# Kernel optimization log

Hardware: AMD Instinct MI355X
Metric: run time of the kernel (lower is better)

Reference implementation:

```python
import jax, jax.numpy as jnp
import numpy as np

G = 128        # number of graphs
N = 512        # nodes per graph
F_IN = 128     # n_feat
H = 128        # agg_hidden
L = 5          # n_layer
FC = 128       # fc_hidden
C = 10         # n_class
E_HALF = 8192  # undirected edge pairs per graph (symmetrized -> 16384 directed)


def setup_inputs() -> dict:
    key = jax.random.key(0)
    ks = jax.random.split(key, 8)
    x = jax.random.normal(ks[0], (G * N, F_IN), dtype=jnp.float32)
    # per-graph random edges, offset into the block-diagonal node index space
    s = jax.random.randint(ks[1], (G, E_HALF), 0, N)
    d = jax.random.randint(ks[2], (G, E_HALF), 0, N)
    off = (jnp.arange(G) * N)[:, None]
    s = (s + off).reshape(-1)
    d = (d + off).reshape(-1)
    src = jnp.concatenate([s, d])  # symmetric adjacency (edges + reversed)
    dst = jnp.concatenate([d, s])
    eps = jnp.zeros((L,), jnp.float32)  # nn.Parameter(torch.zeros(n_layer))
    W = jax.random.normal(ks[3], (L, H, H), jnp.float32) / jnp.sqrt(H)
    b = jnp.zeros((L, H), jnp.float32)
    fc1_w = jax.random.normal(ks[4], (H, FC), jnp.float32) / jnp.sqrt(H)
    fc1_b = jnp.zeros((FC,), jnp.float32)
    fc2_w = jax.random.normal(ks[5], (FC, C), jnp.float32) / jnp.sqrt(FC)
    fc2_b = jnp.zeros((C,), jnp.float32)
    return {"x": x, "eps": eps, "W": W, "b": b,
            "fc1_w": fc1_w, "fc1_b": fc1_b, "fc2_w": fc2_w, "fc2_b": fc2_b,
            "src": src, "dst": dst}


def reference(x, eps, W, b, fc1_w, fc1_b, fc2_w, fc2_b, src, dst):
    n = x.shape[0]
    h = x
    for i in range(L):
        # sparse Adj @ h : gather along src, scatter-add to dst
        pooled = jax.ops.segment_sum(h[src], dst, num_segments=n)
        h = jax.nn.relu(((1.0 + eps[i]) * h + pooled) @ W[i] + b[i])
        # dropout p=0.0 / eval mode -> identity
    hg = h.reshape(G, N, -1).sum(axis=1)          # sum readout over nodes
    hg = jax.nn.relu(hg @ fc1_w + fc1_b)
    return jax.nn.softmax(hg @ fc2_w + fc2_b, axis=-1)
```

## Files before the change

kernel.cpp:

```cpp
#include <hip/hip_runtime.h>

#define NODES 65536
#define GNUM  128
#define NPG   512
#define FDIM  128

#define OFF_A   0u
#define OFF_WT  (16u<<20)
#define OFF_HTA (17u<<20)
#define OFF_HTB (33u<<20)

typedef short bf16x8 __attribute__((ext_vector_type(8)));
typedef float f32x4  __attribute__((ext_vector_type(4)));
typedef unsigned short u16;

#define GLB_AS __attribute__((address_space(1)))
#define LDS_AS __attribute__((address_space(3)))

static __device__ inline void gload16(const void* g, void* l) {
    __builtin_amdgcn_global_load_lds((const GLB_AS unsigned*)g,
                                     (LDS_AS unsigned*)l, 16, 0, 0);
}

static __device__ inline unsigned bf1(float x) {
    unsigned b = __float_as_uint(x);
    return (b + 0x7fffu + ((b >> 16) & 1u)) >> 16;
}
static __device__ inline unsigned pack_bf2(float x, float y) {
    return bf1(x) | (bf1(y) << 16);
}
static __device__ inline bf16x8 cvt8n(unsigned x) {
    union { bf16x8 v; unsigned u[4]; } r;
#pragma unroll
    for (int i = 0; i < 4; ++i) {
        float f0 = (float)((x >> (8 * i)) & 0xFu);
        float f1 = (float)((x >> (8 * i + 4)) & 0xFu);
        r.u[i] = (__float_as_uint(f0) >> 16) | (__float_as_uint(f1) & 0xffff0000u);
    }
    return r.v;
}

__global__ __launch_bounds__(256) void k_cvtT(const float* __restrict__ x,
                                              u16* __restrict__ hT) {
    __shared__ char Cs[128 * 144];
    int t = threadIdx.x;
    int m0 = blockIdx.x * 64;
    int g = m0 >> 9, ml0 = m0 & 511;
#pragma unroll
    for (int it = 0; it < 8; ++it) {
        int i = t + 256 * it;
        int nl = i >> 5, fq = i & 31;
        float4 v = *(const float4*)(x + (size_t)(m0 + nl) * FDIM + fq * 4);
        *(u16*)(Cs + (fq * 4 + 0) * 144 + nl * 2) = (u16)bf1(v.x);
        *(u16*)(Cs + (fq * 4 + 1) * 144 + nl * 2) = (u16)bf1(v.y);
        *(u16*)(Cs + (fq * 4 + 2) * 144 + nl * 2) = (u16)bf1(v.z);
        *(u16*)(Cs + (fq * 4 + 3) * 144 + nl * 2) = (u16)bf1(v.w);
    }
    __syncthreads();
    u16* hg = hT + (size_t)g * 65536 + ml0;
#pragma unroll
    for (int j = 0; j < 4; ++j) {
        int idx = t + 256 * j;
        int f = idx >> 3, piece = idx & 7;
        uint4 v = *(const uint4*)(Cs + f * 144 + piece * 16);
        *(uint4*)((char*)(hg + (size_t)f * 512) + piece * 16) = v;
    }
}

__global__ __launch_bounds__(256) void k_wt(const float* __restrict__ W,
                                            u16* __restrict__ wt) {
    int idx = blockIdx.x * 256 + threadIdx.x;
    int l = idx >> 14, r = idx & 16383;
    int n = r >> 7, k = r & 127;
    wt[idx] = (u16)bf1(W[(l << 14) + k * 128 + n]);
}

__global__ __launch_bounds__(512) void k_adense(const int* __restrict__ src,
                                                const int* __restrict__ dst,
                                                unsigned* __restrict__ A4,
                                                int halfE) {
    __shared__ unsigned cnt[128 * 64];
    int g = blockIdx.x >> 2, dq = blockIdx.x & 3;
    int t = threadIdx.x;
    for (int i = t; i < 128 * 64; i += 512) cnt[i] = 0u;
    __syncthreads();
    int dlo = dq * 128;
    int epg = halfE / GNUM;
#pragma unroll
    for (int r = 0; r < 2; ++r) {
        int base = r * halfE + g * epg;
        const int4* s4 = (const int4*)(src + base);
        const int4* d4 = (const int4*)(dst + base);
        for (int i = t; i < epg / 4; i += 512) {
            int4 sv = s4[i], dv = d4[i];
            int s, dl;
            s = sv.x & (NPG - 1); dl = (dv.x & (NPG - 1)) - dlo;
            if ((unsigned)dl < 128u) atomicAdd(&cnt[dl * 64 + (s >> 3)], 1u << ((s & 7) * 4));
            s = sv.y & (NPG - 1); dl = (dv.y & (NPG - 1)) - dlo;
            if ((unsigned)dl < 128u) atomicAdd(&cnt[dl * 64 + (s >> 3)], 1u << ((s & 7) * 4));
            s = sv.z & (NPG - 1); dl = (dv.z & (NPG - 1)) - dlo;
            if ((unsigned)dl < 128u) atomicAdd(&cnt[dl * 64 + (s >> 3)], 1u << ((s & 7) * 4));
            s = sv.w & (NPG - 1); dl = (dv.w & (NPG - 1)) - dlo;
            if ((unsigned)dl < 128u) atomicAdd(&cnt[dl * 64 + (s >> 3)], 1u << ((s & 7) * 4));
        }
    }
    __syncthreads();
    uint4* Ao = (uint4*)(A4 + ((size_t)g * 512 + dlo) * 64);
    const uint4* ls = (const uint4*)cnt;
    for (int i = t; i < 128 * 16; i += 512) Ao[i] = ls[i];
}

__global__ __launch_bounds__(512, 4) void k_layer(const u16* __restrict__ hT,
                                                  u16* __restrict__ hTo,
                                                  const unsigned char* __restrict__ A,
                                                  const u16* __restrict__ wt,
                                                  const float* __restrict__ bias,
                                                  const float* __restrict__ eps) {
    __shared__ uint4 smem16[75776 / 16];
    char* smem = (char*)smem16;
    char* Ps = smem + 40960;
    int t = threadIdx.x;
    int w = t >> 6, lane = t & 63;
    int q = lane >> 4, ln = lane & 15;
    int g = blockIdx.x & 127, dq = blockIdx.x >> 7;
    const unsigned char* Ab = A + (size_t)g * (512 * 256) + (size_t)dq * 128 * 256;
    const u16* hb = hT + (size_t)g * 65536;

    int pA = w * 64 + lane;
    int rowA = pA >> 1;
    const unsigned char* gA = Ab + rowA * 256 + (pA & 1) * 16;
    int pB0 = w * 128 + lane, pB1 = pB0 + 64;
    int fB0 = pB0 >> 3, fB1 = pB1 >> 3;
    const char* gB0 = (const char*)hb + (size_t)fB0 * 1024 + (((pB0 & 7) ^ (fB0 & 7)) << 4);
    const char* gB1 = (const char*)hb + (size_t)fB1 * 1024 + (((pB1 & 7) ^ (fB1 & 7)) << 4);

    f32x4 acc[8];
#pragma unroll
    for (int nt = 0; nt < 8; ++nt) acc[nt] = (f32x4){0.f, 0.f, 0.f, 0.f};

    int rA = w * 16 + ln;
    if (w < 4) gload16(gA, smem + pA * 16);
    gload16(gB0, smem + 8192 + pB0 * 16);
    gload16(gB1, smem + 8192 + pB1 * 16);
    __syncthreads();
    for (int ch = 0; ch < 8; ++ch) {
        char* Asc = smem + (ch & 1) * 4096;
        char* Bsc = smem + 8192 + (ch & 1) * 16384;
        if (ch < 7) {
            char* Asn = smem + ((ch + 1) & 1) * 4096;
            char* Bsn = smem + 8192 + ((ch + 1) & 1) * 16384;
            if (w < 4) gload16(gA + (ch + 1) * 32, Asn + pA * 16);
            gload16(gB0 + (ch + 1) * 128, Bsn + pB0 * 16);
            gload16(gB1 + (ch + 1) * 128, Bsn + pB1 * 16);
        }
#pragma unroll
        for (int kcL = 0; kcL < 2; ++kcL) {
            unsigned a4 = *(const unsigned*)(Asc + rA * 32 + kcL * 16 + q * 4);
            bf16x8 af = cvt8n(a4);
#pragma unroll
            for (int nt = 0; nt < 8; ++nt) {
                int f = nt * 16 + ln;
                int sB = f * 8 + ((kcL * 4 + q) ^ (f & 7));
                bf16x8 bf = *(const bf16x8*)(Bsc + sB * 16);
                acc[nt] = __builtin_amdgcn_mfma_f32_16x16x32_bf16(af, bf, acc[nt], 0, 0, 0);
            }
        }
        __syncthreads();
    }
    float ep = 1.f + eps[0];
    int rl0 = w * 16 + q * 4;
    int mb0 = dq * 128 + rl0;
#pragma unroll
    for (int nt = 0; nt < 8; ++nt) {
        int f = nt * 16 + ln;
        uint2 sv = *(const uint2*)(hb + (size_t)f * 512 + mb0);
        float s0 = __uint_as_float(sv.x << 16);
        float s1 = __uint_as_float(sv.x & 0xffff0000u);
        float s2 = __uint_as_float(sv.y << 16);
        float s3 = __uint_as_float(sv.y & 0xffff0000u);
        f32x4 a = acc[nt];
        *(u16*)(Ps + (rl0 + 0) * 272 + f * 2) = (u16)bf1(fmaf(ep, s0, a[0]));
        *(u16*)(Ps + (rl0 + 1) * 272 + f * 2) = (u16)bf1(fmaf(ep, s1, a[1]));
        *(u16*)(Ps + (rl0 + 2) * 272 + f * 2) = (u16)bf1(fmaf(ep, s2, a[2]));
        *(u16*)(Ps + (rl0 + 3) * 272 + f * 2) = (u16)bf1(fmaf(ep, s3, a[3]));
    }
    __syncthreads();
    f32x4 acc2[8];
#pragma unroll
    for (int nt = 0; nt < 8; ++nt) acc2[nt] = (f32x4){0.f, 0.f, 0.f, 0.f};
#pragma unroll
    for (int ks = 0; ks < 4; ++ks) {
        bf16x8 af = *(const bf16x8*)(Ps + rA * 272 + ks * 64 + q * 16);
#pragma unroll
        for (int nt = 0; nt < 8; ++nt) {
            bf16x8 bf = *(const bf16x8*)(wt + (size_t)(nt * 16 + ln) * 128 + ks * 32 + q * 8);
            acc2[nt] = __builtin_amdgcn_mfma_f32_16x16x32_bf16(af, bf, acc2[nt], 0, 0, 0);
        }
    }
    __syncthreads();
#pragma unroll
    for (int nt = 0; nt < 8; ++nt) {
        int n = nt * 16 + ln;
        float bv = bias[n];
        f32x4 a = acc2[nt];
        *(uint2*)(Ps + n * 272 + rl0 * 2) =
            make_uint2(pack_bf2(fmaxf(a[0] + bv, 0.f), fmaxf(a[1] + bv, 0.f)),
                       pack_bf2(fmaxf(a[2] + bv, 0.f), fmaxf(a[3] + bv, 0.f)));
    }
    __syncthreads();
    u16* ho = hTo + (size_t)g * 65536 + dq * 128;
#pragma unroll
    for (int j = 0; j < 4; ++j) {
        int idx = t + 512 * j;
        int f = idx >> 4, piece = idx & 15;
        uint4 v = *(const uint4*)(Ps + f * 272 + piece * 16);
        *(uint4*)((char*)(ho + (size_t)f * 512) + piece * 16) = v;
    }
}

__global__ __launch_bounds__(128) void k_r(const u16* __restrict__ hT,
                                           const float* __restrict__ fc1w,
                                           const float* __restrict__ fc1b,
                                           const float* __restrict__ fc2w,
                                           const float* __restrict__ fc2b,
                                           float* __restrict__ out) {
    __shared__ float hg[128], z[128], lg[10];
    int g = blockIdx.x, t = threadIdx.x;
    const uint4* row = (const uint4*)(hT + (size_t)g * 65536 + (size_t)t * 512);
    float acc = 0.f;
#pragma unroll 4
    for (int i = 0; i < 64; ++i) {
        uint4 u = row[i];
        acc += __uint_as_float(u.x << 16) + __uint_as_float(u.x & 0xffff0000u);
        acc += __uint_as_float(u.y << 16) + __uint_as_float(u.y & 0xffff0000u);
        acc += __uint_as_float(u.z << 16) + __uint_as_float(u.z & 0xffff0000u);
        acc += __uint_as_float(u.w << 16) + __uint_as_float(u.w & 0xffff0000u);
    }
    hg[t] = acc;
    __syncthreads();
    float a1 = fc1b[t];
#pragma unroll 4
    for (int k = 0; k < 128; ++k) a1 = fmaf(hg[k], fc1w[k * 128 + t], a1);
    z[t] = fmaxf(a1, 0.f);
    __syncthreads();
    if (t < 10) {
        float l2 = fc2b[t];
        for (int k = 0; k < 128; ++k) l2 = fmaf(z[k], fc2w[k * 10 + t], l2);
        lg[t] = l2;
    }
    __syncthreads();
    if (t < 10) {
        float m = lg[0];
        for (int c = 1; c < 10; ++c) m = fmaxf(m, lg[c]);
        float ssum = 0.f;
        for (int c = 0; c < 10; ++c) ssum += expf(lg[c] - m);
        out[g * 10 + t] = expf(lg[t] - m) / ssum;
    }
}

extern "C" void kernel_launch(void* const* d_in, const int* in_sizes, int n_in,
                              void* d_out, int out_size, void* d_ws, size_t ws_size,
                              hipStream_t stream) {
    const float* x    = (const float*)d_in[0];
    const float* eps  = (const float*)d_in[1];
    const float* W    = (const float*)d_in[2];
    const float* b    = (const float*)d_in[3];
    const float* fc1w = (const float*)d_in[4];
    const float* fc1b = (const float*)d_in[5];
    const float* fc2w = (const float*)d_in[6];
    const float* fc2b = (const float*)d_in[7];
    const int*   src  = (const int*)d_in[8];
    const int*   dst  = (const int*)d_in[9];
    int E = in_sizes[8];
    int halfE = E >> 1;

    char* ws  = (char*)d_ws;
    unsigned char* Abuf = (unsigned char*)(ws + OFF_A);
    u16*  wtb = (u16*)(ws + OFF_WT);
    u16*  hta = (u16*)(ws + OFF_HTA);
    u16*  htb = (u16*)(ws + OFF_HTB);
    float* out = (float*)d_out;

    k_cvtT<<<NODES / 64, 256, 0, stream>>>(x, hta);
    k_wt<<<5 * 128 * 128 / 256, 256, 0, stream>>>(W, wtb);
    k_adense<<<GNUM * 4, 512, 0, stream>>>(src, dst, (unsigned*)Abuf, halfE);

    u16* cur = hta;
    u16* nxt = htb;
    for (int l = 0; l < 5; ++l) {
        k_layer<<<GNUM * 4, 512, 0, stream>>>(cur, nxt, Abuf,
                                              wtb + l * 128 * 128, b + l * 128, eps + l);
        u16* tmp = cur; cur = nxt; nxt = tmp;
    }
    k_r<<<GNUM, 128, 0, stream>>>(cur, fc1w, fc1b, fc2w, fc2b, out);
}
```

Baseline: 292.4 us.

## Halve layer-kernel waves with 2 row tiles each; build adjacency one block per graph

```diff
diff --git a/kernel.cpp b/kernel.cpp
--- a/kernel.cpp
+++ b/kernel.cpp
@@ -75,42 +75,41 @@
     wt[idx] = (u16)bf1(W[(l << 14) + k * 128 + n]);
 }
 
-__global__ __launch_bounds__(512) void k_adense(const int* __restrict__ src,
-                                                const int* __restrict__ dst,
-                                                unsigned* __restrict__ A4,
-                                                int halfE) {
-    __shared__ unsigned cnt[128 * 64];
-    int g = blockIdx.x >> 2, dq = blockIdx.x & 3;
+__global__ __launch_bounds__(1024) void k_adense(const int* __restrict__ src,
+                                                 const int* __restrict__ dst,
+                                                 unsigned* __restrict__ A4,
+                                                 int halfE) {
+    __shared__ uint4 cnt4[512 * 16];
+    unsigned* cnt = (unsigned*)cnt4;
+    int g = blockIdx.x;
     int t = threadIdx.x;
-    for (int i = t; i < 128 * 64; i += 512) cnt[i] = 0u;
-    __syncthreads();
-    int dlo = dq * 128;
+#pragma unroll
+    for (int j = 0; j < 8; ++j) cnt4[t + 1024 * j] = make_uint4(0u, 0u, 0u, 0u);
+    __syncthreads();
     int epg = halfE / GNUM;
 #pragma unroll
     for (int r = 0; r < 2; ++r) {
         int base = r * halfE + g * epg;
         const int4* s4 = (const int4*)(src + base);
         const int4* d4 = (const int4*)(dst + base);
-        for (int i = t; i < epg / 4; i += 512) {
+#pragma unroll
+        for (int it = 0; it < 2; ++it) {
+            int i = t + 1024 * it;
             int4 sv = s4[i], dv = d4[i];
-            int s, dl;
-            s = sv.x & (NPG - 1); dl = (dv.x & (NPG - 1)) - dlo;
-            if ((unsigned)dl < 128u) atomicAdd(&cnt[dl * 64 + (s >> 3)], 1u << ((s & 7) * 4));
-            s = sv.y & (NPG - 1); dl = (dv.y & (NPG - 1)) - dlo;
-            if ((unsigned)dl < 128u) atomicAdd(&cnt[dl * 64 + (s >> 3)], 1u << ((s & 7) * 4));
-            s = sv.z & (NPG - 1); dl = (dv.z & (NPG - 1)) - dlo;
-            if ((unsigned)dl < 128u) atomicAdd(&cnt[dl * 64 + (s >> 3)], 1u << ((s & 7) * 4));
-            s = sv.w & (NPG - 1); dl = (dv.w & (NPG - 1)) - dlo;
-            if ((unsigned)dl < 128u) atomicAdd(&cnt[dl * 64 + (s >> 3)], 1u << ((s & 7) * 4));
-        }
-    }
-    __syncthreads();
-    uint4* Ao = (uint4*)(A4 + ((size_t)g * 512 + dlo) * 64);
-    const uint4* ls = (const uint4*)cnt;
-    for (int i = t; i < 128 * 16; i += 512) Ao[i] = ls[i];
-}
-
-__global__ __launch_bounds__(512, 4) void k_layer(const u16* __restrict__ hT,
+            int s, d;
+            s = sv.x & 511; d = dv.x & 511; atomicAdd(&cnt[d * 64 + (s >> 3)], 1u << ((s & 7) * 4));
+            s = sv.y & 511; d = dv.y & 511; atomicAdd(&cnt[d * 64 + (s >> 3)], 1u << ((s & 7) * 4));
+            s = sv.z & 511; d = dv.z & 511; atomicAdd(&cnt[d * 64 + (s >> 3)], 1u << ((s & 7) * 4));
+            s = sv.w & 511; d = dv.w & 511; atomicAdd(&cnt[d * 64 + (s >> 3)], 1u << ((s & 7) * 4));
+        }
+    }
+    __syncthreads();
+    uint4* Ao = (uint4*)(A4 + (size_t)g * 512 * 64);
+#pragma unroll
+    for (int j = 0; j < 8; ++j) Ao[t + 1024 * j] = cnt4[t + 1024 * j];
+}
+
+__global__ __launch_bounds__(256, 2) void k_layer(const u16* __restrict__ hT,
                                                   u16* __restrict__ hTo,
                                                   const unsigned char* __restrict__ A,
                                                   const u16* __restrict__ wt,
@@ -126,92 +125,110 @@
     const unsigned char* Ab = A + (size_t)g * (512 * 256) + (size_t)dq * 128 * 256;
     const u16* hb = hT + (size_t)g * 65536;
 
-    int pA = w * 64 + lane;
+    int pA = t;
     int rowA = pA >> 1;
     const unsigned char* gA = Ab + rowA * 256 + (pA & 1) * 16;
-    int pB0 = w * 128 + lane, pB1 = pB0 + 64;
-    int fB0 = pB0 >> 3, fB1 = pB1 >> 3;
-    const char* gB0 = (const char*)hb + (size_t)fB0 * 1024 + (((pB0 & 7) ^ (fB0 & 7)) << 4);
-    const char* gB1 = (const char*)hb + (size_t)fB1 * 1024 + (((pB1 & 7) ^ (fB1 & 7)) << 4);
-
-    f32x4 acc[8];
-#pragma unroll
-    for (int nt = 0; nt < 8; ++nt) acc[nt] = (f32x4){0.f, 0.f, 0.f, 0.f};
-
-    int rA = w * 16 + ln;
-    if (w < 4) gload16(gA, smem + pA * 16);
-    gload16(gB0, smem + 8192 + pB0 * 16);
-    gload16(gB1, smem + 8192 + pB1 * 16);
-    __syncthreads();
+    f32x4 acc[2][8];
+#pragma unroll
+    for (int mt = 0; mt < 2; ++mt)
+#pragma unroll
+        for (int nt = 0; nt < 8; ++nt) acc[mt][nt] = (f32x4){0.f, 0.f, 0.f, 0.f};
+
+    gload16(gA, smem + pA * 16);
+#pragma unroll
+    for (int j = 0; j < 4; ++j) {
+        int p = t + 256 * j; int f = p >> 3;
+        gload16((const char*)hb + (size_t)f * 1024 + (((p & 7) ^ (f & 7)) << 4),
+                smem + 8192 + p * 16);
+    }
+    __syncthreads();
+    int rA0 = w * 32 + ln;
     for (int ch = 0; ch < 8; ++ch) {
         char* Asc = smem + (ch & 1) * 4096;
         char* Bsc = smem + 8192 + (ch & 1) * 16384;
         if (ch < 7) {
             char* Asn = smem + ((ch + 1) & 1) * 4096;
             char* Bsn = smem + 8192 + ((ch + 1) & 1) * 16384;
-            if (w < 4) gload16(gA + (ch + 1) * 32, Asn + pA * 16);
-            gload16(gB0 + (ch + 1) * 128, Bsn + pB0 * 16);
-            gload16(gB1 + (ch + 1) * 128, Bsn + pB1 * 16);
+            gload16(gA + (ch + 1) * 32, Asn + pA * 16);
+#pragma unroll
+            for (int j = 0; j < 4; ++j) {
+                int p = t + 256 * j; int f = p >> 3;
+                gload16((const char*)hb + (size_t)f * 1024 + (ch + 1) * 128
+                            + (((p & 7) ^ (f & 7)) << 4),
+                        Bsn + p * 16);
+            }
         }
 #pragma unroll
         for (int kcL = 0; kcL < 2; ++kcL) {
-            unsigned a4 = *(const unsigned*)(Asc + rA * 32 + kcL * 16 + q * 4);
-            bf16x8 af = cvt8n(a4);
+            bf16x8 af0 = cvt8n(*(const unsigned*)(Asc + rA0 * 32 + kcL * 16 + q * 4));
+            bf16x8 af1 = cvt8n(*(const unsigned*)(Asc + (rA0 + 16) * 32 + kcL * 16 + q * 4));
 #pragma unroll
             for (int nt = 0; nt < 8; ++nt) {
                 int f = nt * 16 + ln;
                 int sB = f * 8 + ((kcL * 4 + q) ^ (f & 7));
                 bf16x8 bf = *(const bf16x8*)(Bsc + sB * 16);
-                acc[nt] = __builtin_amdgcn_mfma_f32_16x16x32_bf16(af, bf, acc[nt], 0, 0, 0);
+                acc[0][nt] = __builtin_amdgcn_mfma_f32_16x16x32_bf16(af0, bf, acc[0][nt], 0, 0, 0);
+                acc[1][nt] = __builtin_amdgcn_mfma_f32_16x16x32_bf16(af1, bf, acc[1][nt], 0, 0, 0);
             }
         }
         __syncthreads();
     }
     float ep = 1.f + eps[0];
-    int rl0 = w * 16 + q * 4;
-    int mb0 = dq * 128 + rl0;
-#pragma unroll
-    for (int nt = 0; nt < 8; ++nt) {
-        int f = nt * 16 + ln;
-        uint2 sv = *(const uint2*)(hb + (size_t)f * 512 + mb0);
-        float s0 = __uint_as_float(sv.x << 16);
-        float s1 = __uint_as_float(sv.x & 0xffff0000u);
-        float s2 = __uint_as_float(sv.y << 16);
-        float s3 = __uint_as_float(sv.y & 0xffff0000u);
-        f32x4 a = acc[nt];
-        *(u16*)(Ps + (rl0 + 0) * 272 + f * 2) = (u16)bf1(fmaf(ep, s0, a[0]));
-        *(u16*)(Ps + (rl0 + 1) * 272 + f * 2) = (u16)bf1(fmaf(ep, s1, a[1]));
-        *(u16*)(Ps + (rl0 + 2) * 272 + f * 2) = (u16)bf1(fmaf(ep, s2, a[2]));
-        *(u16*)(Ps + (rl0 + 3) * 272 + f * 2) = (u16)bf1(fmaf(ep, s3, a[3]));
-    }
-    __syncthreads();
-    f32x4 acc2[8];
-#pragma unroll
-    for (int nt = 0; nt < 8; ++nt) acc2[nt] = (f32x4){0.f, 0.f, 0.f, 0.f};
+#pragma unroll
+    for (int mt = 0; mt < 2; ++mt) {
+        int rl0 = w * 32 + mt * 16 + q * 4;
+        int mb0 = dq * 128 + rl0;
+#pragma unroll
+        for (int nt = 0; nt < 8; ++nt) {
+            int f = nt * 16 + ln;
+            uint2 sv = *(const uint2*)(hb + (size_t)f * 512 + mb0);
+            float s0 = __uint_as_float(sv.x << 16);
+            float s1 = __uint_as_float(sv.x & 0xffff0000u);
+            float s2 = __uint_as_float(sv.y << 16);
+            float s3 = __uint_as_float(sv.y & 0xffff0000u);
+            f32x4 a = acc[mt][nt];
+            *(u16*)(Ps + (rl0 + 0) * 272 + f * 2) = (u16)bf1(fmaf(ep, s0, a[0]));
+            *(u16*)(Ps + (rl0 + 1) * 272 + f * 2) = (u16)bf1(fmaf(ep, s1, a[1]));
+            *(u16*)(Ps + (rl0 + 2) * 272 + f * 2) = (u16)bf1(fmaf(ep, s2, a[2]));
+            *(u16*)(Ps + (rl0 + 3) * 272 + f * 2) = (u16)bf1(fmaf(ep, s3, a[3]));
+        }
+    }
+    __syncthreads();
+    f32x4 acc2[2][8];
+#pragma unroll
+    for (int mt = 0; mt < 2; ++mt)
+#pragma unroll
+        for (int nt = 0; nt < 8; ++nt) acc2[mt][nt] = (f32x4){0.f, 0.f, 0.f, 0.f};
 #pragma unroll
     for (int ks = 0; ks < 4; ++ks) {
-        bf16x8 af = *(const bf16x8*)(Ps + rA * 272 + ks * 64 + q * 16);
+        bf16x8 af0 = *(const bf16x8*)(Ps + rA0 * 272 + ks * 64 + q * 16);
+        bf16x8 af1 = *(const bf16x8*)(Ps + (rA0 + 16) * 272 + ks * 64 + q * 16);
 #pragma unroll
         for (int nt = 0; nt < 8; ++nt) {
             bf16x8 bf = *(const bf16x8*)(wt + (size_t)(nt * 16 + ln) * 128 + ks * 32 + q * 8);
-            acc2[nt] = __builtin_amdgcn_mfma_f32_16x16x32_bf16(af, bf, acc2[nt], 0, 0, 0);
-        }
-    }
-    __syncthreads();
-#pragma unroll
-    for (int nt = 0; nt < 8; ++nt) {
-        int n = nt * 16 + ln;
-        float bv = bias[n];
-        f32x4 a = acc2[nt];
-        *(uint2*)(Ps + n * 272 + rl0 * 2) =
-            make_uint2(pack_bf2(fmaxf(a[0] + bv, 0.f), fmaxf(a[1] + bv, 0.f)),
-                       pack_bf2(fmaxf(a[2] + bv, 0.f), fmaxf(a[3] + bv, 0.f)));
+            acc2[0][nt] = __builtin_amdgcn_mfma_f32_16x16x32_bf16(af0, bf, acc2[0][nt], 0, 0, 0);
+            acc2[1][nt] = __builtin_amdgcn_mfma_f32_16x16x32_bf16(af1, bf, acc2[1][nt], 0, 0, 0);
+        }
+    }
+    __syncthreads();
+#pragma unroll
+    for (int mt = 0; mt < 2; ++mt) {
+        int rl0 = w * 32 + mt * 16 + q * 4;
+#pragma unroll
+        for (int nt = 0; nt < 8; ++nt) {
+            int n = nt * 16 + ln;
+            float bv = bias[n];
+            f32x4 a = acc2[mt][nt];
+            *(uint2*)(Ps + n * 272 + rl0 * 2) =
+                make_uint2(pack_bf2(fmaxf(a[0] + bv, 0.f), fmaxf(a[1] + bv, 0.f)),
+                           pack_bf2(fmaxf(a[2] + bv, 0.f), fmaxf(a[3] + bv, 0.f)));
+        }
     }
     __syncthreads();
     u16* ho = hTo + (size_t)g * 65536 + dq * 128;
 #pragma unroll
-    for (int j = 0; j < 4; ++j) {
-        int idx = t + 512 * j;
+    for (int j = 0; j < 8; ++j) {
+        int idx = t + 256 * j;
         int f = idx >> 4, piece = idx & 15;
         uint4 v = *(const uint4*)(Ps + f * 272 + piece * 16);
         *(uint4*)((char*)(ho + (size_t)f * 512) + piece * 16) = v;
@@ -283,12 +300,12 @@
 
     k_cvtT<<<NODES / 64, 256, 0, stream>>>(x, hta);
     k_wt<<<5 * 128 * 128 / 256, 256, 0, stream>>>(W, wtb);
-    k_adense<<<GNUM * 4, 512, 0, stream>>>(src, dst, (unsigned*)Abuf, halfE);
+    k_adense<<<GNUM, 1024, 0, stream>>>(src, dst, (unsigned*)Abuf, halfE);
 
     u16* cur = hta;
     u16* nxt = htb;
     for (int l = 0; l < 5; ++l) {
-        k_layer<<<GNUM * 4, 512, 0, stream>>>(cur, nxt, Abuf,
+        k_layer<<<GNUM * 4, 256, 0, stream>>>(cur, nxt, Abuf,
                                               wtb + l * 128 * 128, b + l * 128, eps + l);
         u16* tmp = cur; cur = nxt; nxt = tmp;
     }
```

Result: faster. 244.1 us (-16.5%).
